# Optimization experiments

Measured on AMD Instinct MI355X. Metric: run time of the kernel, lower is better.

The kernel has to match this reference:

```python
import jax, jax.numpy as jnp
import numpy as np

D = 1024
H = 16
DK = D // H


def setup_inputs() -> dict:
    key = jax.random.key(0)
    ks = jax.random.split(key, 10)
    B, S = 2, 2048
    scale = 1.0 / np.sqrt(D)
    inp = {
        "x": jax.random.normal(ks[0], (B, S, D), dtype=jnp.float32),
        "mask": jax.random.randint(ks[1], (B, S), 0, 2, dtype=jnp.int32),
        "wq": jax.random.normal(ks[2], (D, D), dtype=jnp.float32) * scale,
        "bq": jnp.zeros((D,), dtype=jnp.float32),
        "wk": jax.random.normal(ks[3], (D, D), dtype=jnp.float32) * scale,
        "bk": jnp.zeros((D,), dtype=jnp.float32),
        "wv": jax.random.normal(ks[4], (D, D), dtype=jnp.float32) * scale,
        "bv": jnp.zeros((D,), dtype=jnp.float32),
        "wo": jax.random.normal(ks[5], (D, D), dtype=jnp.float32) * scale,
        "bo": jnp.zeros((D,), dtype=jnp.float32),
    }
    return inp


def reference(x, mask, wq, bq, wk, bk, wv, bv, wo, bo):
    B, S, _ = x.shape
    # torch Linear: y = x @ W.T + b
    def proj(w, b):
        return (jnp.einsum("bsd,ed->bse", x, w) + b).reshape(B, S, H, DK).transpose(0, 2, 1, 3)  # (B,H,S,dk)

    q = proj(wq, bq)
    k = proj(wk, bk)
    v = proj(wv, bv)

    scores = jnp.einsum("bhqd,bhkd->bhqk", q, k) / jnp.sqrt(jnp.float32(DK))  # (B,H,S,S)
    # original: mask.unsqueeze(1).unsqueeze(3) -> (B,1,S,1), masks along the QUERY axis
    m = mask[:, None, :, None]  # (B,1,S,1)
    scores = jnp.where(m == 0, jnp.float32(-1e9), scores)
    attn = jax.nn.softmax(scores, axis=-1)
    ctx = jnp.einsum("bhqk,bhkd->bhqd", attn, v)  # (B,H,S,dk)
    concat = ctx.transpose(0, 2, 1, 3).reshape(B, S, D)
    return jnp.einsum("bsd,ed->bse", concat, wo) + bo
```

## Files before the change

kernel.cpp:

```cpp
#include <hip/hip_runtime.h>
#include <hip/hip_bf16.h>

#define SEQ 2048
#define DM  1024

typedef __attribute__((ext_vector_type(8))) _Float16 f16x8;
typedef __attribute__((ext_vector_type(4)))  float   f32x4;

#define EXP2F(x) __builtin_amdgcn_exp2f(x)

__device__ __forceinline__ ushort f2h(float x) {
    union { _Float16 h; ushort u; } c; c.h = (_Float16)x; return c.u;
}
__device__ __forceinline__ unsigned pk2h(float a, float b) {
    typedef __fp16 fp16v2 __attribute__((ext_vector_type(2)));
    union { fp16v2 h; unsigned u; } c;
    c.h = __builtin_amdgcn_cvt_pkrtz(a, b);
    return c.u;
}

__device__ __forceinline__ void gload16(const void* g, void* l) {
    __builtin_amdgcn_global_load_lds(
        (const __attribute__((address_space(1))) unsigned*)(uintptr_t)g,
        (__attribute__((address_space(3))) unsigned*)(uintptr_t)l, 16, 0, 0);
}

__global__ __launch_bounds__(256)
void cvt_all(const float* __restrict__ x,  const float* __restrict__ wq,
             const float* __restrict__ wk, const float* __restrict__ wv,
             const float* __restrict__ wo,
             ushort* __restrict__ xH, ushort* __restrict__ wH)
{
    const int NX4 = (2 * SEQ * DM) / 4;
    const int NW4 = (DM * DM) / 4;
    const int total = NX4 + 4 * NW4;
    for (int i = blockIdx.x * 256 + threadIdx.x; i < total; i += gridDim.x * 256) {
        float4 v; ushort4* dst;
        if (i < NX4) {
            v = ((const float4*)x)[i];
            dst = (ushort4*)xH + i;
        } else {
            const int j = i - NX4;
            const int wi = j >> 18;
            const int jo = j & (NW4 - 1);
            const float* ws_ = (wi == 0) ? wq : (wi == 1) ? wk : (wi == 2) ? wv : wo;
            v = ((const float4*)ws_)[jo];
            dst = (ushort4*)wH + j;
        }
        ushort4 h;
        h.x = f2h(v.x); h.y = f2h(v.y); h.z = f2h(v.z); h.w = f2h(v.w);
        *dst = h;
    }
}

template<int BM, int BN, int WM, int WN, int MODE>
__global__ __launch_bounds__(WM * WN * 64)
void gemm5(const ushort* __restrict__ A, const ushort* __restrict__ B,
           const float* __restrict__ b0, const float* __restrict__ b1,
           const float* __restrict__ b2,
           ushort* __restrict__ QH, ushort* __restrict__ KH,
           ushort* __restrict__ VH, float* __restrict__ outf, int nmt)
{
    constexpr int NW  = WM * WN;
    constexpr int PR  = BM / WM, PC = BN / WN;
    constexpr int MR  = PR / 16, NR = PC / 16, MH = MR / 2;
    constexpr int APW = (BM / 8) / NW;
    constexpr int BPW = (BN / 8) / NW;
    constexpr int NT  = DM / 64;

    __shared__ ushort A_lds[2][BM * 64];
    __shared__ ushort B_lds[2][BN * 64];

    const int tid = threadIdx.x, w = tid >> 6, lane = tid & 63;
    const int nwg = gridDim.x, q8 = nwg >> 3;
    const int wg  = (blockIdx.x & 7) * q8 + (blockIdx.x >> 3);
    const int m0  = (wg % nmt) * BM, n0 = (wg / nmt) * BN;
    const int wm  = w / WN, wn = w % WN;

    auto stage = [&](int buf, int kt) {
        const int k0 = kt * 64;
#pragma unroll
        for (int j = 0; j < APW; ++j) {
            const int s   = w * APW + j;
            const int row = s * 8 + (lane >> 3);
            const int cl  = (lane & 7) ^ (row & 7);
            gload16(A + (size_t)(m0 + row) * DM + k0 + cl * 8,
                    &A_lds[buf][s * 512]);
        }
#pragma unroll
        for (int j = 0; j < BPW; ++j) {
            const int s   = w * BPW + j;
            const int row = s * 8 + (lane >> 3);
            const int cl  = (lane & 7) ^ (row & 7);
            gload16(B + (size_t)(n0 + row) * DM + k0 + cl * 8,
                    &B_lds[buf][s * 512]);
        }
    };

    f32x4 acc[MR][NR];
#pragma unroll
    for (int i = 0; i < MR; ++i)
#pragma unroll
        for (int j = 0; j < NR; ++j) acc[i][j] = f32x4{0.f, 0.f, 0.f, 0.f};

    stage(0, 0);
    stage(1, 1);

    for (int t = 0; t < NT; ++t) {
        const int buf = t & 1;
        if (t == NT - 1) asm volatile("s_waitcnt vmcnt(0)" ::: "memory");
        else             asm volatile("s_waitcnt vmcnt(8)" ::: "memory");
        __builtin_amdgcn_sched_barrier(0);
        __builtin_amdgcn_s_barrier();

        f16x8 bf_[NR][2];
#pragma unroll
        for (int nf = 0; nf < NR; ++nf) {
            const int r = wn * PC + nf * 16 + (lane & 15);
#pragma unroll
            for (int kb = 0; kb < 2; ++kb) {
                const int c = kb * 4 + (lane >> 4);
                bf_[nf][kb] = *(const f16x8*)&B_lds[buf][r * 64 + ((c ^ (r & 7)) << 3)];
            }
        }
#pragma unroll
        for (int qm = 0; qm < 2; ++qm) {
            f16x8 af_[MH][2];
#pragma unroll
            for (int mf = 0; mf < MH; ++mf) {
                const int r = wm * PR + qm * (PR / 2) + mf * 16 + (lane & 15);
#pragma unroll
                for (int kb = 0; kb < 2; ++kb) {
                    const int c = kb * 4 + (lane >> 4);
                    af_[mf][kb] = *(const f16x8*)&A_lds[buf][r * 64 + ((c ^ (r & 7)) << 3)];
                }
            }
            __builtin_amdgcn_s_setprio(1);
#pragma unroll
            for (int kb = 0; kb < 2; ++kb)
#pragma unroll
                for (int mf = 0; mf < MH; ++mf)
#pragma unroll
                    for (int nf = 0; nf < NR; ++nf)
                        acc[qm * MH + mf][nf] = __builtin_amdgcn_mfma_f32_16x16x32_f16(
                            af_[mf][kb], bf_[nf][kb], acc[qm * MH + mf][nf], 0, 0, 0);
            __builtin_amdgcn_s_setprio(0);
        }
        __builtin_amdgcn_sched_barrier(0);
        __builtin_amdgcn_s_barrier();
        __builtin_amdgcn_sched_barrier(0);
        if (t + 2 < NT) stage(buf, t + 2);
    }

#pragma unroll
    for (int mf = 0; mf < MR; ++mf)
#pragma unroll
        for (int nf = 0; nf < NR; ++nf) {
            const int col  = n0 + wn * PC + nf * 16 + (lane & 15);
            const int row0 = m0 + wm * PR + mf * 16 + ((lane >> 4) << 2);
            f32x4 v = acc[mf][nf];
            if constexpr (MODE == 1) {
                float4 o;
                o.x = v[0] + b0[row0 + 0];
                o.y = v[1] + b0[row0 + 1];
                o.z = v[2] + b0[row0 + 2];
                o.w = v[3] + b0[row0 + 3];
                *(float4*)&outf[(size_t)col * DM + row0] = o;
            } else {
                const int sel = row0 >> 10;
                const int e = row0 & 1023;
                const int b = col >> 11, s = col & 2047;
                const int h = e >> 6, dk = e & 63;
                const float* bp = (sel == 0) ? b0 : (sel == 1) ? b1 : b2;
                const float sc = (sel == 0) ? 0.125f * 1.44269504089f : 1.0f;
                const float v0 = (v[0] + bp[e + 0]) * sc;
                const float v1 = (v[1] + bp[e + 1]) * sc;
                const float v2 = (v[2] + bp[e + 2]) * sc;
                const float v3 = (v[3] + bp[e + 3]) * sc;
                const int bh = b * 16 + h;
                ushort4 hv;
                hv.x = f2h(v0); hv.y = f2h(v1); hv.z = f2h(v2); hv.w = f2h(v3);
                if (sel == 0) {
                    const size_t off = ((size_t)bh * SEQ + s) * 64 + dk;
                    *(ushort4*)&QH[off] = hv;
                } else if (sel == 1) {
                    const size_t off = ((size_t)bh * SEQ + s) * 64 + dk;
                    *(ushort4*)&KH[off] = hv;
                } else {
                    const size_t o0 = ((size_t)bh * 64 + dk) * SEQ + s;
                    VH[o0]           = hv.x;
                    VH[o0 + SEQ]     = hv.y;
                    VH[o0 + 2 * SEQ] = hv.z;
                    VH[o0 + 3 * SEQ] = hv.w;
                }
            }
        }
}

__global__ __launch_bounds__(512, 2)
void attn_k(const ushort* __restrict__ QH, const ushort* __restrict__ KH,
            const ushort* __restrict__ VH, const int* __restrict__ mask,
            ushort* __restrict__ ch)
{
    __shared__ ushort Ks[4][64 * 64];
    __shared__ ushort Vs[4][64 * 64];
    __shared__ ushort Ps[8][16 * 64];

    const int t = threadIdx.x, w = t >> 6, lane = t & 63;
    const int wg = (blockIdx.x & 7) * 64 + (blockIdx.x >> 3);
    const int bh = wg >> 4, qt = wg & 15;
    const int b = bh >> 4, h = bh & 15;
    const int q0 = qt * 128 + w * 16;
    const size_t base = (size_t)bh * SEQ * 64;
    const int lq = lane & 15, cb = lane >> 4;

    const int msk = mask[b * SEQ + q0 + lq];
    f16x8 qf[2];
#pragma unroll
    for (int kb = 0; kb < 2; ++kb) {
        qf[kb] = *(const f16x8*)&QH[base + (size_t)(q0 + lq) * 64 + kb * 32 + cb * 8];
        if (msk == 0) qf[kb] = f16x8{0, 0, 0, 0, 0, 0, 0, 0};
    }

    float l_part = 0.f;
    f32x4 acc[4];
#pragma unroll
    for (int df = 0; df < 4; ++df) acc[df] = f32x4{0.f, 0.f, 0.f, 0.f};

    f16x8 sK0, sV0, sK1, sV1;
    const int sr = t >> 3, scc = t & 7;
    const int wr_off = sr * 64 + (scc ^ (sr & 7)) * 8;
    const ushort* gK = &KH[base + (size_t)sr * 64 + scc * 8];
    const ushort* gV = &VH[base + (size_t)sr * SEQ + scc * 8];
    auto load_pair = [&]() {
        sK0 = *(const f16x8*)gK; gK += 4096;
        sV0 = *(const f16x8*)gV; gV += 64;
        sK1 = *(const f16x8*)gK; gK += 4096;
        sV1 = *(const f16x8*)gV; gV += 64;
    };

    load_pair();
    *(f16x8*)&Ks[0][wr_off] = sK0;  *(f16x8*)&Vs[0][wr_off] = sV0;
    *(f16x8*)&Ks[1][wr_off] = sK1;  *(f16x8*)&Vs[1][wr_off] = sV1;
    load_pair();
    __syncthreads();

    auto compute = [&](const int BUF) {
        f32x4 st[4];
#pragma unroll
        for (int mf = 0; mf < 4; ++mf) st[mf] = f32x4{0.f, 0.f, 0.f, 0.f};
        __builtin_amdgcn_s_setprio(1);
#pragma unroll
        for (int mf = 0; mf < 4; ++mf) {
            const int r = mf * 16 + lq;
#pragma unroll
            for (int kb = 0; kb < 2; ++kb) {
                const int p = (kb * 4 + cb) ^ (r & 7);
                f16x8 kf = *(const f16x8*)&Ks[BUF][r * 64 + p * 8];
                st[mf] = __builtin_amdgcn_mfma_f32_16x16x32_f16(kf, qf[kb], st[mf], 0, 0, 0);
            }
        }
        __builtin_amdgcn_s_setprio(0);

#pragma unroll
        for (int mf = 0; mf < 2; ++mf) {
            const float e0 = EXP2F(st[mf][0]);
            const float e1 = EXP2F(st[mf][1]);
            const float e2 = EXP2F(st[mf][2]);
            const float e3 = EXP2F(st[mf][3]);
            l_part += (e0 + e1) + (e2 + e3);
            uint2 pw;
            pw.x = pk2h(e0, e1);
            pw.y = pk2h(e2, e3);
            const int key0 = mf * 16 + (cb << 2);
            const int p = (key0 >> 3) ^ (lq & 7);
            *(uint2*)&Ps[w][lq * 64 + p * 8 + (key0 & 7)] = pw;
        }
        {
            const int p0 = cb ^ (lq & 7);
            f16x8 pf0 = *(const f16x8*)&Ps[w][lq * 64 + p0 * 8];
            __builtin_amdgcn_s_setprio(1);
#pragma unroll
            for (int df = 0; df < 4; ++df) {
                const int r = df * 16 + lq;
                const int p = cb ^ (r & 7);
                f16x8 vf = *(const f16x8*)&Vs[BUF][r * 64 + p * 8];
                acc[df] = __builtin_amdgcn_mfma_f32_16x16x32_f16(vf, pf0, acc[df], 0, 0, 0);
            }
            __builtin_amdgcn_s_setprio(0);
        }
#pragma unroll
        for (int mf = 2; mf < 4; ++mf) {
            const float e0 = EXP2F(st[mf][0]);
            const float e1 = EXP2F(st[mf][1]);
            const float e2 = EXP2F(st[mf][2]);
            const float e3 = EXP2F(st[mf][3]);
            l_part += (e0 + e1) + (e2 + e3);
            uint2 pw;
            pw.x = pk2h(e0, e1);
            pw.y = pk2h(e2, e3);
            const int key0 = mf * 16 + (cb << 2);
            const int p = (key0 >> 3) ^ (lq & 7);
            *(uint2*)&Ps[w][lq * 64 + p * 8 + (key0 & 7)] = pw;
        }
        {
            const int p1 = (4 + cb) ^ (lq & 7);
            f16x8 pf1 = *(const f16x8*)&Ps[w][lq * 64 + p1 * 8];
            __builtin_amdgcn_s_setprio(1);
#pragma unroll
            for (int df = 0; df < 4; ++df) {
                const int r = df * 16 + lq;
                const int p = (4 + cb) ^ (r & 7);
                f16x8 vf = *(const f16x8*)&Vs[BUF][r * 64 + p * 8];
                acc[df] = __builtin_amdgcn_mfma_f32_16x16x32_f16(vf, pf1, acc[df], 0, 0, 0);
            }
            __builtin_amdgcn_s_setprio(0);
        }
    };

    auto step = [&](const int PH, const bool WR, const bool LD) {
        if (WR) {
            const int w0 = PH ? 0 : 2, w1 = PH ? 1 : 3;
            *(f16x8*)&Ks[w0][wr_off] = sK0;  *(f16x8*)&Vs[w0][wr_off] = sV0;
            *(f16x8*)&Ks[w1][wr_off] = sK1;  *(f16x8*)&Vs[w1][wr_off] = sV1;
        }
        if (LD) load_pair();
        compute(PH ? 2 : 0);
        compute(PH ? 3 : 1);
        __builtin_amdgcn_sched_barrier(0);
        asm volatile("s_waitcnt lgkmcnt(0)" ::: "memory");
        __builtin_amdgcn_s_barrier();
        __builtin_amdgcn_sched_barrier(0);
    };

#pragma unroll 1
    for (int i = 0; i < 7; ++i) {
        step(0, true, true);
        step(1, true, true);
    }
    step(0, true, false);
    step(1, false, false);

    {
        float l_tot = l_part;
        l_tot += __shfl_xor(l_tot, 16);
        l_tot += __shfl_xor(l_tot, 32);
        const float inv = 1.0f / l_tot;
        const int s = q0 + lq;
#pragma unroll
        for (int df = 0; df < 4; ++df) {
            const int e0 = h * 64 + df * 16 + (cb << 2);
            ushort4 hv;
            hv.x = f2h(acc[df][0] * inv);
            hv.y = f2h(acc[df][1] * inv);
            hv.z = f2h(acc[df][2] * inv);
            hv.w = f2h(acc[df][3] * inv);
            *(ushort4*)&ch[(size_t)(b * SEQ + s) * DM + e0] = hv;
        }
    }
}

extern "C" void kernel_launch(void* const* d_in, const int* in_sizes, int n_in,
                              void* d_out, int out_size, void* d_ws, size_t ws_size,
                              hipStream_t stream)
{
    const float* x  = (const float*)d_in[0];
    const int* mask = (const int*)d_in[1];
    const float* wq = (const float*)d_in[2];
    const float* bq = (const float*)d_in[3];
    const float* wk = (const float*)d_in[4];
    const float* bk = (const float*)d_in[5];
    const float* wv = (const float*)d_in[6];
    const float* bv = (const float*)d_in[7];
    const float* wo = (const float*)d_in[8];
    const float* bo = (const float*)d_in[9];
    float* out = (float*)d_out;

    const size_t M1 = 1024 * 1024;
    ushort* W = (ushort*)d_ws;
    ushort* xH = W;
    ushort* wH = W + 4 * M1;
    ushort* QH = W + 8 * M1;
    ushort* KH = W + 12 * M1;
    ushort* VH = W + 16 * M1;

    cvt_all<<<2048, 256, 0, stream>>>(x, wq, wk, wv, wo, xH, wH);

    gemm5<384, 128, 4, 2, 0><<<256, 512, 0, stream>>>(
        wH, xH, bq, bk, bv, QH, KH, VH, nullptr, 8);

    attn_k<<<512, 512, 0, stream>>>(QH, KH, VH, mask, xH);

    gemm5<128, 128, 2, 2, 1><<<256, 256, 0, stream>>>(
        wH + 3 * M1, xH, bo, nullptr, nullptr,
        nullptr, nullptr, nullptr, out, 8);
}
```

Before: 104.3 us.

## Stream K/V tiles directly into LDS with global_load_lds and vmcnt pipelining

The attention kernel's K/V staging no longer loads tiles into registers and then writes them to LDS. It now issues global_load_lds direct-to-LDS copies, with the XOR swizzle applied on the global source address. The loop is restructured so each step waits on vmcnt for the older pair of buffers, barriers, computes, then barriers again before refilling the freed buffers. This removes the VGPR round trip and the ds_write instructions but adds an extra barrier per step and relies on the precise vmcnt accounting.

```diff
diff --git a/kernel.cpp b/kernel.cpp
--- a/kernel.cpp
+++ b/kernel.cpp
@@ -227,23 +227,20 @@
 #pragma unroll
     for (int df = 0; df < 4; ++df) acc[df] = f32x4{0.f, 0.f, 0.f, 0.f};
 
-    f16x8 sK0, sV0, sK1, sV1;
-    const int sr = t >> 3, scc = t & 7;
-    const int wr_off = sr * 64 + (scc ^ (sr & 7)) * 8;
-    const ushort* gK = &KH[base + (size_t)sr * 64 + scc * 8];
-    const ushort* gV = &VH[base + (size_t)sr * SEQ + scc * 8];
-    auto load_pair = [&]() {
-        sK0 = *(const f16x8*)gK; gK += 4096;
-        sV0 = *(const f16x8*)gV; gV += 64;
-        sK1 = *(const f16x8*)gK; gK += 4096;
-        sV1 = *(const f16x8*)gV; gV += 64;
+    const int srow = w * 8 + (lane >> 3);
+    const int scl  = (lane & 7) ^ (srow & 7);
+    const ushort* gK = &KH[base + (size_t)srow * 64 + scl * 8];
+    const ushort* gV = &VH[base + (size_t)srow * SEQ + scl * 8];
+    const int wbase = w * 512;
+    auto issue_pair = [&](const int B0, const int B1) {
+        gload16(gK, &Ks[B0][wbase]); gK += 4096;
+        gload16(gV, &Vs[B0][wbase]); gV += 64;
+        gload16(gK, &Ks[B1][wbase]); gK += 4096;
+        gload16(gV, &Vs[B1][wbase]); gV += 64;
     };
 
-    load_pair();
-    *(f16x8*)&Ks[0][wr_off] = sK0;  *(f16x8*)&Vs[0][wr_off] = sV0;
-    *(f16x8*)&Ks[1][wr_off] = sK1;  *(f16x8*)&Vs[1][wr_off] = sV1;
-    load_pair();
-    __syncthreads();
+    issue_pair(0, 1);
+    issue_pair(2, 3);
 
     auto compute = [&](const int BUF) {
         f32x4 st[4];
@@ -318,28 +315,29 @@
         }
     };
 
-    auto step = [&](const int PH, const bool WR, const bool LD) {
-        if (WR) {
-            const int w0 = PH ? 0 : 2, w1 = PH ? 1 : 3;
-            *(f16x8*)&Ks[w0][wr_off] = sK0;  *(f16x8*)&Vs[w0][wr_off] = sV0;
-            *(f16x8*)&Ks[w1][wr_off] = sK1;  *(f16x8*)&Vs[w1][wr_off] = sV1;
-        }
-        if (LD) load_pair();
+    auto step = [&](const int PH, const bool ISSUE, const bool LAST) {
+        if (LAST) asm volatile("s_waitcnt vmcnt(0)" ::: "memory");
+        else      asm volatile("s_waitcnt vmcnt(4)" ::: "memory");
+        __builtin_amdgcn_sched_barrier(0);
+        __builtin_amdgcn_s_barrier();
         compute(PH ? 2 : 0);
         compute(PH ? 3 : 1);
-        __builtin_amdgcn_sched_barrier(0);
-        asm volatile("s_waitcnt lgkmcnt(0)" ::: "memory");
-        __builtin_amdgcn_s_barrier();
-        __builtin_amdgcn_sched_barrier(0);
+        if (ISSUE) {
+            __builtin_amdgcn_sched_barrier(0);
+            asm volatile("s_waitcnt lgkmcnt(0)" ::: "memory");
+            __builtin_amdgcn_s_barrier();
+            __builtin_amdgcn_sched_barrier(0);
+            if (PH) issue_pair(2, 3); else issue_pair(0, 1);
+        }
     };
 
 #pragma unroll 1
     for (int i = 0; i < 7; ++i) {
-        step(0, true, true);
-        step(1, true, true);
-    }
-    step(0, true, false);
-    step(1, false, false);
+        step(0, true, false);
+        step(1, true, false);
+    }
+    step(0, false, false);
+    step(1, false, true);
 
     {
         float l_tot = l_part;
```

Result: no change. 103.4 us (-0.8%).
